# Performance work log

Measured on AMD Instinct MI355X. Metric: run time of the kernel, lower is better.

Reference implementation:

```python
import jax, jax.numpy as jnp
import numpy as np

N_GRAPHS = 500
CHAIN = 200
D_STATE = 64
HID = 128
NEG_SLOPE = 0.2  # PyG GATConv default


def setup_inputs() -> dict:
    key = jax.random.key(0)
    ks = jax.random.split(key, 9)
    N = N_GRAPHS * CHAIN
    # batched bidirectional chain graphs (as in create_chain_graph_batch)
    off = np.arange(N_GRAPHS, dtype=np.int32) * CHAIN
    a = (off[:, None] + np.arange(CHAIN - 1, dtype=np.int32)[None, :]).ravel()
    b = a + 1
    edge_index = jnp.asarray(np.stack([np.concatenate([a, b]), np.concatenate([b, a])]), dtype=jnp.int32)
    x = jax.random.normal(ks[0], (N, D_STATE), jnp.float32)
    s1 = 1.0 / np.sqrt(D_STATE)
    W1 = jax.random.normal(ks[1], (D_STATE, 2 * HID), jnp.float32) * s1
    att_src1 = jax.random.normal(ks[2], (2, HID), jnp.float32) * (1.0 / np.sqrt(HID))
    att_dst1 = jax.random.normal(ks[3], (2, HID), jnp.float32) * (1.0 / np.sqrt(HID))
    b1 = jnp.zeros((2 * HID,), jnp.float32)
    s2 = 1.0 / np.sqrt(2 * HID)
    W2 = jax.random.normal(ks[4], (2 * HID, HID), jnp.float32) * s2
    att_src2 = jax.random.normal(ks[5], (1, HID), jnp.float32) * (1.0 / np.sqrt(HID))
    att_dst2 = jax.random.normal(ks[6], (1, HID), jnp.float32) * (1.0 / np.sqrt(HID))
    b2 = jnp.zeros((HID,), jnp.float32)
    return {"x": x, "edge_index": edge_index, "W1": W1, "att_src1": att_src1,
            "att_dst1": att_dst1, "b1": b1, "W2": W2, "att_src2": att_src2,
            "att_dst2": att_dst2, "b2": b2}


def gat_conv(x, src, dst, W, att_src, att_dst, bias, concat):
    # PyG GATConv: per-head linear, additive attention, segment softmax over dst
    N = x.shape[0]
    H, C = att_src.shape
    h = (x @ W).reshape(N, H, C)                          # [N,H,C]
    a_s = (h * att_src).sum(-1)                           # [N,H]
    a_d = (h * att_dst).sum(-1)                           # [N,H]
    logits = jax.nn.leaky_relu(a_s[src] + a_d[dst], NEG_SLOPE)  # [E,H]
    m = jax.ops.segment_max(logits, dst, num_segments=N)
    e = jnp.exp(logits - m[dst])
    s = jax.ops.segment_sum(e, dst, num_segments=N)
    alpha = e / (s[dst] + 1e-16)                          # [E,H]
    out = jax.ops.segment_sum(h[src] * alpha[:, :, None], dst, num_segments=N)  # [N,H,C]
    out = out.reshape(N, H * C) if concat else out.mean(axis=1)
    return out + bias


def reference(x, edge_index, W1, att_src1, att_dst1, b1, W2, att_src2, att_dst2, b2):
    N = x.shape[0]
    loop = jnp.arange(N, dtype=edge_index.dtype)
    src = jnp.concatenate([edge_index[0], loop])  # add_self_loops=True (PyG default)
    dst = jnp.concatenate([edge_index[1], loop])
    h = gat_conv(x, src, dst, W1, att_src1, att_dst1, b1, concat=True)
    h = jax.nn.gelu(h, approximate=False)  # torch F.gelu default = exact erf
    h = gat_conv(h, src, dst, W2, att_src2, att_dst2, b2, concat=False)
    return jax.nn.gelu(h, approximate=False)
```

## Files before the change

kernel.cpp:

```cpp
#include <hip/hip_runtime.h>
#include <hip/hip_bf16.h>

#define NG 500
#define CH 200
#define NN (NG*CH)
#define DS 64
#define HDIM 128
#define C1 256
#define NEG_SLOPE 0.2f
#define GB 1563

typedef unsigned short ushort_t;
typedef __attribute__((ext_vector_type(8))) short bf16x8;
typedef __attribute__((ext_vector_type(4))) float f32x4;

__device__ __forceinline__ float us2f(ushort_t u){
  union { unsigned int i; float f; } v; v.i = ((unsigned int)u) << 16; return v.f;
}
__device__ __forceinline__ ushort_t f2us(float f){
  union { float f; unsigned int i; } v; v.f = f;
  unsigned int x = v.i;
  return (ushort_t)((x + 0x7fffu + ((x >> 16) & 1u)) >> 16);
}
__device__ __forceinline__ float lrelu(float v){ return v > 0.f ? v : NEG_SLOPE * v; }
__device__ __forceinline__ float gelu_fast(float x){
  float x2 = x * x;
  float z  = x * fmaf(0.0713548162726f, x2, 1.59576912161f);
  float e  = __expf(-z);
  return x / fmaf(e, 1.f, 1.f) ;
}

__global__ void probe_dtype(const void* __restrict__ x, int* __restrict__ flag){
  __shared__ int cnt;
  if (threadIdx.x == 0) cnt = 0;
  __syncthreads();
  const ushort_t* p = (const ushort_t*)x;
  int local = 0;
  for (int i = threadIdx.x; i < 8192; i += 256) {
    float v = us2f(p[i]);
    if (!(fabsf(v) < 100.f)) local++;
  }
  atomicAdd(&cnt, local);
  __syncthreads();
  if (threadIdx.x == 0) flag[0] = (cnt > 16) ? 1 : 0;
}

__global__ void prep_w(const int* __restrict__ flag,
                       const void* W1, const void* as1, const void* ad1, const void* b1,
                       const void* W2, const void* as2, const void* ad2, const void* b2,
                       ushort_t* w1t, ushort_t* w2t,
                       float* asrc1f, float* adst1f, float* b1f,
                       float* asrc2f, float* adst2f, float* b2f)
{
  const bool F = flag[0] != 0;
  int i = blockIdx.x * 256 + threadIdx.x;
  #define LD(p, j) (F ? ((const float*)(p))[j] : us2f(((const ushort_t*)(p))[j]))
  if (i < 16384)      { int k = i >> 8, n = i & 255; w1t[n*64  + k] = f2us(LD(W1, i)); }
  else if (i < 49152) { int j = i - 16384, k = j >> 7, n = j & 127; w2t[n*256 + k] = f2us(LD(W2, j)); }
  else if (i < 49408) { asrc1f[i-49152] = LD(as1, i-49152); }
  else if (i < 49664) { adst1f[i-49408] = LD(ad1, i-49408); }
  else if (i < 49920) { b1f[i-49664]    = LD(b1,  i-49664); }
  else if (i < 50048) { asrc2f[i-49920] = LD(as2, i-49920); }
  else if (i < 50176) { adst2f[i-50048] = LD(ad2, i-50048); }
  else if (i < 50304) { b2f[i-50176]    = LD(b2,  i-50176); }
  #undef LD
}

__global__ __launch_bounds__(256, 4) void fused(
    const int* __restrict__ flag, const void* __restrict__ x,
    const ushort_t* __restrict__ w1t, const ushort_t* __restrict__ w2t,
    const float* __restrict__ asrc1f, const float* __restrict__ adst1f, const float* __restrict__ b1f,
    const float* __restrict__ asrc2f, const float* __restrict__ adst2f, const float* __restrict__ b2f,
    void* __restrict__ out)
{
  __shared__ ushort_t lds[17952];
  __shared__ float part_s[4][68], part_d[4][68];
  __shared__ float alp[66*8];
  ushort_t* As  = lds;
  ushort_t* g1L = lds;

  const int t  = threadIdx.x;
  const int m0 = blockIdx.x * 64;
  const int l = t & 63, w = t >> 6;
  const int ln = l & 15, quad = l >> 4;
  const bool F = flag[0] != 0;

  #pragma unroll
  for (int i = 0; i < 5; i++) {
    int q = t + i*256;
    int r = q >> 4, off = (q & 15) * 4;
    int gr = m0 - 2 + r;
    ushort4 v = {0,0,0,0};
    if (r < 68 && gr >= 0 && gr < NN) {
      if (F) {
        float4 xv = *(const float4*)(&((const float*)x)[(size_t)gr*DS + off]);
        v.x = f2us(xv.x); v.y = f2us(xv.y); v.z = f2us(xv.z); v.w = f2us(xv.w);
      } else {
        v = *(const ushort4*)(&((const ushort_t*)x)[(size_t)gr*DS + off]);
      }
    }
    *(ushort4*)(&As[r*72 + off]) = v;
  }

  f32x4 acc[5][4];
  #pragma unroll
  for (int mi = 0; mi < 5; mi++)
    #pragma unroll
    for (int nj = 0; nj < 4; nj++) acc[mi][nj] = (f32x4){0.f,0.f,0.f,0.f};

  __syncthreads();
  #pragma unroll
  for (int h = 0; h < 2; h++) {
    #pragma unroll
    for (int ks = 0; ks < 2; ks++) {
      const int kk = ks*32 + quad*8;
      bf16x8 a[5], b[2];
      #pragma unroll
      for (int njl = 0; njl < 2; njl++)
        b[njl] = *(const bf16x8*)(&w1t[(w*64 + h*32 + njl*16 + ln)*64 + kk]);
      #pragma unroll
      for (int mi = 0; mi < 5; mi++) a[mi] = *(const bf16x8*)(&As[(mi*16 + ln)*72 + kk]);
      #pragma unroll
      for (int mi = 0; mi < 5; mi++)
        #pragma unroll
        for (int njl = 0; njl < 2; njl++)
          acc[mi][2*h+njl] = __builtin_amdgcn_mfma_f32_16x16x32_bf16(a[mi], b[njl], acc[mi][2*h+njl], 0, 0, 0);
    }
  }

  {
    float wsv[4], wdv[4];
    #pragma unroll
    for (int nj = 0; nj < 4; nj++) {
      wsv[nj] = asrc1f[w*64 + nj*16 + ln];
      wdv[nj] = adst1f[w*64 + nj*16 + ln];
    }
    #pragma unroll
    for (int mi = 0; mi < 5; mi++)
      #pragma unroll
      for (int r = 0; r < 4; r++) {
        float s = 0.f, d = 0.f;
        #pragma unroll
        for (int nj = 0; nj < 4; nj++) { s += acc[mi][nj][r] * wsv[nj]; d += acc[mi][nj][r] * wdv[nj]; }
        #pragma unroll
        for (int o = 1; o < 16; o <<= 1) { s += __shfl_xor(s, o, 64); d += __shfl_xor(d, o, 64); }
        int row = mi*16 + quad*4 + r;
        if (ln == 0 && row < 68) { part_s[w][row] = s; part_d[w][row] = d; }
      }
  }
  __syncthreads();

  if (t < 132) {
    int hh = (t >= 66) ? 1 : 0;
    int n  = t - 66*hh;
    int gj = m0 - 1 + n;
    int p  = gj % CH;
    float ad   = part_d[2*hh][n+1] + part_d[2*hh+1][n+1];
    float as_s = part_s[2*hh][n+1] + part_s[2*hh+1][n+1];
    float as_l = part_s[2*hh][n  ] + part_s[2*hh+1][n  ];
    float as_r = part_s[2*hh][n+2] + part_s[2*hh+1][n+2];
    bool hl = p > 0, hr = p < CH-1;
    float zs = lrelu(as_s + ad);
    float zl = hl ? lrelu(as_l + ad) : -1e30f;
    float zr = hr ? lrelu(as_r + ad) : -1e30f;
    float mx = fmaxf(zs, fmaxf(zl, zr));
    float el = hl ? __expf(zl - mx) : 0.f;
    float es = __expf(zs - mx);
    float er = hr ? __expf(zr - mx) : 0.f;
    float inv = 1.f / (el + es + er + 1e-16f);
    alp[n*8 + hh*4 + 0] = el*inv; alp[n*8 + hh*4 + 1] = es*inv; alp[n*8 + hh*4 + 2] = er*inv;
  }
  __syncthreads();

  {
    float b1v[4];
    #pragma unroll
    for (int nj = 0; nj < 4; nj++) b1v[nj] = b1f[w*64 + nj*16 + ln];
    if (t < 132) {
      int rr = (t < 66) ? 0 : 67;
      int c4 = ((t < 66) ? t : t - 66) * 4;
      ushort4 z = {0,0,0,0};
      *(ushort4*)(&g1L[rr*264 + c4]) = z;
    }
    const int head = w >> 1;
    #pragma unroll
    for (int mi = 0; mi < 5; mi++) {
      const int mip = (mi < 4) ? mi+1 : 4;
      const int mim = (mi > 0) ? mi-1 : 0;
      float hp3[4], hm0[4];
      #pragma unroll
      for (int nj = 0; nj < 4; nj++) {
        float up_a = __shfl(acc[mi ][nj][0], (l+16)&63, 64);
        float up_b = __shfl(acc[mip][nj][0], (l+16)&63, 64);
        float dn_a = __shfl(acc[mi ][nj][3], (l-16)&63, 64);
        float dn_b = __shfl(acc[mim][nj][3], (l-16)&63, 64);
        hp3[nj] = (quad < 3) ? up_a : up_b;
        hm0[nj] = (quad > 0) ? dn_a : dn_b;
      }
      #pragma unroll
      for (int r = 0; r < 4; r++) {
        int row = mi*16 + quad*4 + r;
        if (row >= 1 && row <= 66) {
          float4 av = *(const float4*)(&alp[(row-1)*8 + head*4]);
          #pragma unroll
          for (int nj = 0; nj < 4; nj++) {
            float self = acc[mi][nj][r];
            float hm = (r > 0) ? acc[mi][nj][r-1] : hm0[nj];
            float hp = (r < 3) ? acc[mi][nj][r+1] : hp3[nj];
            float v = av.y*self + av.x*hm + av.z*hp + b1v[nj];
            g1L[row*264 + w*64 + nj*16 + ln] = f2us(gelu_fast(v));
          }
        }
      }
    }
  }
  __syncthreads();

  f32x4 acc2[5][2];
  #pragma unroll
  for (int mi = 0; mi < 5; mi++)
    #pragma unroll
    for (int nj = 0; nj < 2; nj++) acc2[mi][nj] = (f32x4){0.f,0.f,0.f,0.f};

  #pragma unroll
  for (int ck = 0; ck < 4; ck++) {
    bf16x8 a2[2][5];
    #pragma unroll
    for (int ks = 0; ks < 2; ks++)
      #pragma unroll
      for (int mi = 0; mi < 5; mi++) {
        int ar = mi*16 + ln;
        if (mi == 4) ar = (ar < 67) ? ar : 67;
        a2[ks][mi] = *(const bf16x8*)(&g1L[ar*264 + ck*64 + ks*32 + quad*8]);
      }
    #pragma unroll
    for (int h2 = 0; h2 < 2; h2++) {
      #pragma unroll
      for (int ks = 0; ks < 2; ks++) {
        bf16x8 b = *(const bf16x8*)(&w2t[(w*32 + h2*16 + ln)*256 + ck*64 + ks*32 + quad*8]);
        #pragma unroll
        for (int mi = 0; mi < 5; mi++)
          acc2[mi][h2] = __builtin_amdgcn_mfma_f32_16x16x32_bf16(a2[ks][mi], b, acc2[mi][h2], 0, 0, 0);
      }
    }
  }

  {
    float ws2[2], wd2[2];
    #pragma unroll
    for (int nj = 0; nj < 2; nj++) {
      ws2[nj] = asrc2f[w*32 + nj*16 + ln];
      wd2[nj] = adst2f[w*32 + nj*16 + ln];
    }
    #pragma unroll
    for (int mi = 0; mi < 5; mi++)
      #pragma unroll
      for (int r = 0; r < 4; r++) {
        float s = 0.f, d = 0.f;
        #pragma unroll
        for (int nj = 0; nj < 2; nj++) { s += acc2[mi][nj][r] * ws2[nj]; d += acc2[mi][nj][r] * wd2[nj]; }
        #pragma unroll
        for (int o = 1; o < 16; o <<= 1) { s += __shfl_xor(s, o, 64); d += __shfl_xor(d, o, 64); }
        int row = mi*16 + quad*4 + r;
        if (ln == 0 && row < 68) { part_s[w][row] = s; part_d[w][row] = d; }
      }
  }
  __syncthreads();

  if (t < 64) {
    int gi = m0 + t;
    if (gi < NN) {
      int p = gi % CH;
      float ad = 0.f, as_s = 0.f, as_l = 0.f, as_r = 0.f;
      #pragma unroll
      for (int ww = 0; ww < 4; ww++) {
        ad   += part_d[ww][t+2];
        as_s += part_s[ww][t+2];
        as_l += part_s[ww][t+1];
        as_r += part_s[ww][t+3];
      }
      bool hl = p > 0, hr = p < CH-1;
      float zs = lrelu(as_s + ad);
      float zl = hl ? lrelu(as_l + ad) : -1e30f;
      float zr = hr ? lrelu(as_r + ad) : -1e30f;
      float mx = fmaxf(zs, fmaxf(zl, zr));
      float el = hl ? __expf(zl - mx) : 0.f;
      float es = __expf(zs - mx);
      float er = hr ? __expf(zr - mx) : 0.f;
      float inv = 1.f / (el + es + er + 1e-16f);
      alp[t*4 + 0] = el*inv; alp[t*4 + 1] = es*inv; alp[t*4 + 2] = er*inv;
    }
  }
  __syncthreads();

  {
    float b2v[2];
    #pragma unroll
    for (int nj = 0; nj < 2; nj++) b2v[nj] = b2f[w*32 + nj*16 + ln];
    #pragma unroll
    for (int mi = 0; mi < 5; mi++) {
      const int mip = (mi < 4) ? mi+1 : 4;
      const int mim = (mi > 0) ? mi-1 : 0;
      float hp3[2], hm0[2];
      #pragma unroll
      for (int nj = 0; nj < 2; nj++) {
        float up_a = __shfl(acc2[mi ][nj][0], (l+16)&63, 64);
        float up_b = __shfl(acc2[mip][nj][0], (l+16)&63, 64);
        float dn_a = __shfl(acc2[mi ][nj][3], (l-16)&63, 64);
        float dn_b = __shfl(acc2[mim][nj][3], (l-16)&63, 64);
        hp3[nj] = (quad < 3) ? up_a : up_b;
        hm0[nj] = (quad > 0) ? dn_a : dn_b;
      }
      #pragma unroll
      for (int r = 0; r < 4; r++) {
        int row = mi*16 + quad*4 + r;
        if (row >= 2 && row <= 65) {
          int n = row - 2;
          int gi = m0 + n;
          if (gi < NN) {
            float4 av = *(const float4*)(&alp[n*4]);
            #pragma unroll
            for (int nj = 0; nj < 2; nj++) {
              float self = acc2[mi][nj][r];
              float hm = (r > 0) ? acc2[mi][nj][r-1] : hm0[nj];
              float hp = (r < 3) ? acc2[mi][nj][r+1] : hp3[nj];
              float v = av.y*self + av.x*hm + av.z*hp + b2v[nj];
              float o = gelu_fast(v);
              int c2 = w*32 + nj*16 + ln;
              if (F) ((float*)out)[(size_t)gi*HDIM + c2] = o;
              else   ((ushort_t*)out)[(size_t)gi*HDIM + c2] = f2us(o);
            }
          }
        }
      }
    }
  }
}

extern "C" void kernel_launch(void* const* d_in, const int* in_sizes, int n_in,
                              void* d_out, int out_size, void* d_ws, size_t ws_size,
                              hipStream_t stream)
{
  const void* x   = d_in[0];
  const void* W1  = d_in[2];
  const void* as1 = d_in[3];
  const void* ad1 = d_in[4];
  const void* b1  = d_in[5];
  const void* W2  = d_in[6];
  const void* as2 = d_in[7];
  const void* ad2 = d_in[8];
  const void* b2  = d_in[9];

  char* w = (char*)d_ws;
  size_t off = 0;
  int* flag = (int*)w;                       off += 256;
  ushort_t* w1t = (ushort_t*)(w + off);      off += 64 * 256 * 2;
  ushort_t* w2t = (ushort_t*)(w + off);      off += 256 * 128 * 2;
  float* asrc1f = (float*)(w + off);         off += 256 * 4;
  float* adst1f = (float*)(w + off);         off += 256 * 4;
  float* b1f    = (float*)(w + off);         off += 256 * 4;
  float* asrc2f = (float*)(w + off);         off += 128 * 4;
  float* adst2f = (float*)(w + off);         off += 128 * 4;
  float* b2f    = (float*)(w + off);         off += 128 * 4;

  probe_dtype<<<1, 256, 0, stream>>>(x, flag);
  prep_w<<<197, 256, 0, stream>>>(flag, W1, as1, ad1, b1, W2, as2, ad2, b2,
                                  w1t, w2t, asrc1f, adst1f, b1f, asrc2f, adst2f, b2f);
  fused<<<GB, 256, 0, stream>>>(flag, x, w1t, w2t, asrc1f, adst1f, b1f,
                                asrc2f, adst2f, b2f, d_out);
}
```

Measured before the change: 173.6 us.

## Fold attention vectors into weights and compute attention logits via extra MFMA

Precomputes W·att_src and W·att_dst vectors, split into hi/lo bf16 pairs, in the prep kernel. The fused kernel then gets per-node attention logits from an extra MFMA column tile instead of per-lane dot products plus a 16-lane shuffle reduction, and the LDS partial arrays are merged into one scratch buffer. It also uses packed bf16 conversion instructions, rcp intrinsics and a reworked gelu. The trade is extra MFMA work on one wave per K-slice, plus a small precision change from the bf16 hi/lo split and the approximate reciprocal.

```diff
diff --git a/kernel.cpp b/kernel.cpp
--- a/kernel.cpp
+++ b/kernel.cpp
@@ -22,12 +22,17 @@
   unsigned int x = v.i;
   return (ushort_t)((x + 0x7fffu + ((x >> 16) & 1u)) >> 16);
 }
+__device__ __forceinline__ unsigned int cvt_pk_bf16(float a, float b){
+  unsigned int r;
+  asm("v_cvt_pk_bf16_f32 %0, %1, %2" : "=v"(r) : "v"(a), "v"(b));
+  return r;
+}
 __device__ __forceinline__ float lrelu(float v){ return v > 0.f ? v : NEG_SLOPE * v; }
 __device__ __forceinline__ float gelu_fast(float x){
   float x2 = x * x;
-  float z  = x * fmaf(0.0713548162726f, x2, 1.59576912161f);
-  float e  = __expf(-z);
-  return x / fmaf(e, 1.f, 1.f) ;
+  float zn = x * fmaf(-0.0713548163f, x2, -1.5957691216f);
+  float e  = __expf(zn);
+  return x * __builtin_amdgcn_rcpf(1.f + e);
 }
 
 __global__ void probe_dtype(const void* __restrict__ x, int* __restrict__ flag){
@@ -50,7 +55,8 @@
                        const void* W2, const void* as2, const void* ad2, const void* b2,
                        ushort_t* w1t, ushort_t* w2t,
                        float* asrc1f, float* adst1f, float* b1f,
-                       float* asrc2f, float* adst2f, float* b2f)
+                       float* asrc2f, float* adst2f, float* b2f,
+                       ushort_t* wsd1, ushort_t* wsd2)
 {
   const bool F = flag[0] != 0;
   int i = blockIdx.x * 256 + threadIdx.x;
@@ -63,19 +69,41 @@
   else if (i < 50048) { asrc2f[i-49920] = LD(as2, i-49920); }
   else if (i < 50176) { adst2f[i-50048] = LD(ad2, i-50048); }
   else if (i < 50304) { b2f[i-50176]    = LD(b2,  i-50176); }
+  else if (i < 50560) {
+    int j = i - 50304, k = j >> 2, c = j & 3;
+    int head = c >> 1;
+    const void* av = (c & 1) ? ad1 : as1;
+    float s = 0.f;
+    for (int cc = 0; cc < 128; cc++)
+      s += LD(W1, k*256 + head*128 + cc) * LD(av, head*128 + cc);
+    ushort_t hi = f2us(s);
+    wsd1[c*64 + k] = hi;
+    wsd1[(c+4)*64 + k] = f2us(s - us2f(hi));
+  }
+  else if (i < 51072) {
+    int j = i - 50560, k = j >> 1, c = j & 1;
+    const void* av = c ? ad2 : as2;
+    float s = 0.f;
+    for (int cc = 0; cc < 128; cc++)
+      s += LD(W2, k*128 + cc) * LD(av, cc);
+    ushort_t hi = f2us(s);
+    wsd2[c*256 + k] = hi;
+    wsd2[(c+2)*256 + k] = f2us(s - us2f(hi));
+  }
+  else if (i < 51584) { wsd1[512  + (i - 51072)] = 0; }
+  else if (i < 54656) { wsd2[1024 + (i - 51584)] = 0; }
   #undef LD
 }
 
 __global__ __launch_bounds__(256, 4) void fused(
     const int* __restrict__ flag, const void* __restrict__ x,
     const ushort_t* __restrict__ w1t, const ushort_t* __restrict__ w2t,
-    const float* __restrict__ asrc1f, const float* __restrict__ adst1f, const float* __restrict__ b1f,
-    const float* __restrict__ asrc2f, const float* __restrict__ adst2f, const float* __restrict__ b2f,
+    const ushort_t* __restrict__ wsd1, const ushort_t* __restrict__ wsd2,
+    const float* __restrict__ b1f, const float* __restrict__ b2f,
     void* __restrict__ out)
 {
   __shared__ ushort_t lds[17952];
-  __shared__ float part_s[4][68], part_d[4][68];
-  __shared__ float alp[66*8];
+  __shared__ float scratch[800];
   ushort_t* As  = lds;
   ushort_t* g1L = lds;
 
@@ -90,16 +118,18 @@
     int q = t + i*256;
     int r = q >> 4, off = (q & 15) * 4;
     int gr = m0 - 2 + r;
-    ushort4 v = {0,0,0,0};
     if (r < 68 && gr >= 0 && gr < NN) {
       if (F) {
         float4 xv = *(const float4*)(&((const float*)x)[(size_t)gr*DS + off]);
-        v.x = f2us(xv.x); v.y = f2us(xv.y); v.z = f2us(xv.z); v.w = f2us(xv.w);
+        uint2 u; u.x = cvt_pk_bf16(xv.x, xv.y); u.y = cvt_pk_bf16(xv.z, xv.w);
+        *(uint2*)(&As[r*72 + off]) = u;
       } else {
-        v = *(const ushort4*)(&((const ushort_t*)x)[(size_t)gr*DS + off]);
-      }
-    }
-    *(ushort4*)(&As[r*72 + off]) = v;
+        *(ushort4*)(&As[r*72 + off]) = *(const ushort4*)(&((const ushort_t*)x)[(size_t)gr*DS + off]);
+      }
+    } else {
+      ushort4 z = {0,0,0,0};
+      *(ushort4*)(&As[r*72 + off]) = z;
+    }
   }
 
   f32x4 acc[5][4];
@@ -107,6 +137,9 @@
   for (int mi = 0; mi < 5; mi++)
     #pragma unroll
     for (int nj = 0; nj < 4; nj++) acc[mi][nj] = (f32x4){0.f,0.f,0.f,0.f};
+  f32x4 acc_att[5];
+  #pragma unroll
+  for (int mi = 0; mi < 5; mi++) acc_att[mi] = (f32x4){0.f,0.f,0.f,0.f};
 
   __syncthreads();
   #pragma unroll
@@ -125,27 +158,24 @@
         #pragma unroll
         for (int njl = 0; njl < 2; njl++)
           acc[mi][2*h+njl] = __builtin_amdgcn_mfma_f32_16x16x32_bf16(a[mi], b[njl], acc[mi][2*h+njl], 0, 0, 0);
-    }
-  }
-
-  {
-    float wsv[4], wdv[4];
-    #pragma unroll
-    for (int nj = 0; nj < 4; nj++) {
-      wsv[nj] = asrc1f[w*64 + nj*16 + ln];
-      wdv[nj] = adst1f[w*64 + nj*16 + ln];
-    }
+      if (h == 0 && w == 0) {
+        bf16x8 batt = *(const bf16x8*)(&wsd1[ln*64 + kk]);
+        #pragma unroll
+        for (int mi = 0; mi < 5; mi++)
+          acc_att[mi] = __builtin_amdgcn_mfma_f32_16x16x32_bf16(a[mi], batt, acc_att[mi], 0, 0, 0);
+      }
+    }
+  }
+
+  if (w == 0) {
     #pragma unroll
     for (int mi = 0; mi < 5; mi++)
       #pragma unroll
       for (int r = 0; r < 4; r++) {
-        float s = 0.f, d = 0.f;
-        #pragma unroll
-        for (int nj = 0; nj < 4; nj++) { s += acc[mi][nj][r] * wsv[nj]; d += acc[mi][nj][r] * wdv[nj]; }
-        #pragma unroll
-        for (int o = 1; o < 16; o <<= 1) { s += __shfl_xor(s, o, 64); d += __shfl_xor(d, o, 64); }
+        float v = acc_att[mi][r];
+        float vc = v + __shfl(v, (l + 4) & 63, 64);
         int row = mi*16 + quad*4 + r;
-        if (ln == 0 && row < 68) { part_s[w][row] = s; part_d[w][row] = d; }
+        if (ln < 4 && row < 68) scratch[ln*68 + row] = vc;
       }
   }
   __syncthreads();
@@ -155,10 +185,9 @@
     int n  = t - 66*hh;
     int gj = m0 - 1 + n;
     int p  = gj % CH;
-    float ad   = part_d[2*hh][n+1] + part_d[2*hh+1][n+1];
-    float as_s = part_s[2*hh][n+1] + part_s[2*hh+1][n+1];
-    float as_l = part_s[2*hh][n  ] + part_s[2*hh+1][n  ];
-    float as_r = part_s[2*hh][n+2] + part_s[2*hh+1][n+2];
+    const float* Sa = &scratch[(2*hh)*68];
+    const float* Da = &scratch[(2*hh+1)*68];
+    float ad = Da[n+1], as_s = Sa[n+1], as_l = Sa[n], as_r = Sa[n+2];
     bool hl = p > 0, hr = p < CH-1;
     float zs = lrelu(as_s + ad);
     float zl = hl ? lrelu(as_l + ad) : -1e30f;
@@ -167,8 +196,10 @@
     float el = hl ? __expf(zl - mx) : 0.f;
     float es = __expf(zs - mx);
     float er = hr ? __expf(zr - mx) : 0.f;
-    float inv = 1.f / (el + es + er + 1e-16f);
-    alp[n*8 + hh*4 + 0] = el*inv; alp[n*8 + hh*4 + 1] = es*inv; alp[n*8 + hh*4 + 2] = er*inv;
+    float inv = __builtin_amdgcn_rcpf(el + es + er + 1e-16f);
+    scratch[272 + n*8 + hh*4 + 0] = el*inv;
+    scratch[272 + n*8 + hh*4 + 1] = es*inv;
+    scratch[272 + n*8 + hh*4 + 2] = er*inv;
   }
   __syncthreads();
 
@@ -176,9 +207,9 @@
     float b1v[4];
     #pragma unroll
     for (int nj = 0; nj < 4; nj++) b1v[nj] = b1f[w*64 + nj*16 + ln];
-    if (t < 132) {
-      int rr = (t < 66) ? 0 : 67;
-      int c4 = ((t < 66) ? t : t - 66) * 4;
+    if (t < 128) {
+      int rr = (t < 64) ? 0 : 67;
+      int c4 = (t & 63) * 4;
       ushort4 z = {0,0,0,0};
       *(ushort4*)(&g1L[rr*264 + c4]) = z;
     }
@@ -201,15 +232,20 @@
       for (int r = 0; r < 4; r++) {
         int row = mi*16 + quad*4 + r;
         if (row >= 1 && row <= 66) {
-          float4 av = *(const float4*)(&alp[(row-1)*8 + head*4]);
+          float4 av = *(const float4*)(&scratch[272 + (row-1)*8 + head*4]);
+          float o[4];
           #pragma unroll
           for (int nj = 0; nj < 4; nj++) {
             float self = acc[mi][nj][r];
             float hm = (r > 0) ? acc[mi][nj][r-1] : hm0[nj];
             float hp = (r < 3) ? acc[mi][nj][r+1] : hp3[nj];
-            float v = av.y*self + av.x*hm + av.z*hp + b1v[nj];
-            g1L[row*264 + w*64 + nj*16 + ln] = f2us(gelu_fast(v));
+            o[nj] = gelu_fast(av.y*self + av.x*hm + av.z*hp + b1v[nj]);
           }
+          unsigned int u01 = cvt_pk_bf16(o[0], o[1]);
+          unsigned int u23 = cvt_pk_bf16(o[2], o[3]);
+          ushort_t* base = &g1L[row*264 + w*64 + ln];
+          base[0]  = (ushort_t)u01; base[16] = (ushort_t)(u01 >> 16);
+          base[32] = (ushort_t)u23; base[48] = (ushort_t)(u23 >> 16);
         }
       }
     }
@@ -221,6 +257,9 @@
   for (int mi = 0; mi < 5; mi++)
     #pragma unroll
     for (int nj = 0; nj < 2; nj++) acc2[mi][nj] = (f32x4){0.f,0.f,0.f,0.f};
+  f32x4 acc2_att[5];
+  #pragma unroll
+  for (int mi = 0; mi < 5; mi++) acc2_att[mi] = (f32x4){0.f,0.f,0.f,0.f};
 
   #pragma unroll
   for (int ck = 0; ck < 4; ck++) {
@@ -233,6 +272,15 @@
         if (mi == 4) ar = (ar < 67) ? ar : 67;
         a2[ks][mi] = *(const bf16x8*)(&g1L[ar*264 + ck*64 + ks*32 + quad*8]);
       }
+    if (ck == w) {
+      #pragma unroll
+      for (int ks = 0; ks < 2; ks++) {
+        bf16x8 batt2 = *(const bf16x8*)(&wsd2[ln*256 + ck*64 + ks*32 + quad*8]);
+        #pragma unroll
+        for (int mi = 0; mi < 5; mi++)
+          acc2_att[mi] = __builtin_amdgcn_mfma_f32_16x16x32_bf16(a2[ks][mi], batt2, acc2_att[mi], 0, 0, 0);
+      }
+    }
     #pragma unroll
     for (int h2 = 0; h2 < 2; h2++) {
       #pragma unroll
@@ -245,26 +293,15 @@
     }
   }
 
-  {
-    float ws2[2], wd2[2];
-    #pragma unroll
-    for (int nj = 0; nj < 2; nj++) {
-      ws2[nj] = asrc2f[w*32 + nj*16 + ln];
-      wd2[nj] = adst2f[w*32 + nj*16 + ln];
-    }
-    #pragma unroll
-    for (int mi = 0; mi < 5; mi++)
-      #pragma unroll
-      for (int r = 0; r < 4; r++) {
-        float s = 0.f, d = 0.f;
-        #pragma unroll
-        for (int nj = 0; nj < 2; nj++) { s += acc2[mi][nj][r] * ws2[nj]; d += acc2[mi][nj][r] * wd2[nj]; }
-        #pragma unroll
-        for (int o = 1; o < 16; o <<= 1) { s += __shfl_xor(s, o, 64); d += __shfl_xor(d, o, 64); }
-        int row = mi*16 + quad*4 + r;
-        if (ln == 0 && row < 68) { part_s[w][row] = s; part_d[w][row] = d; }
-      }
-  }
+  #pragma unroll
+  for (int mi = 0; mi < 5; mi++)
+    #pragma unroll
+    for (int r = 0; r < 4; r++) {
+      float v = acc2_att[mi][r];
+      float vc = v + __shfl(v, (l + 2) & 63, 64);
+      int row = mi*16 + quad*4 + r;
+      if (ln < 2 && row < 68) scratch[(w*2 + ln)*68 + row] = vc;
+    }
   __syncthreads();
 
   if (t < 64) {
@@ -274,10 +311,10 @@
       float ad = 0.f, as_s = 0.f, as_l = 0.f, as_r = 0.f;
       #pragma unroll
       for (int ww = 0; ww < 4; ww++) {
-        ad   += part_d[ww][t+2];
-        as_s += part_s[ww][t+2];
-        as_l += part_s[ww][t+1];
-        as_r += part_s[ww][t+3];
+        as_s += scratch[(ww*2)*68 + t+2];
+        as_l += scratch[(ww*2)*68 + t+1];
+        as_r += scratch[(ww*2)*68 + t+3];
+        ad   += scratch[(ww*2+1)*68 + t+2];
       }
       bool hl = p > 0, hr = p < CH-1;
       float zs = lrelu(as_s + ad);
@@ -287,8 +324,10 @@
       float el = hl ? __expf(zl - mx) : 0.f;
       float es = __expf(zs - mx);
       float er = hr ? __expf(zr - mx) : 0.f;
-      float inv = 1.f / (el + es + er + 1e-16f);
-      alp[t*4 + 0] = el*inv; alp[t*4 + 1] = es*inv; alp[t*4 + 2] = er*inv;
+      float inv = __builtin_amdgcn_rcpf(el + es + er + 1e-16f);
+      scratch[544 + t*4 + 0] = el*inv;
+      scratch[544 + t*4 + 1] = es*inv;
+      scratch[544 + t*4 + 2] = er*inv;
     }
   }
   __syncthreads();
@@ -318,17 +357,28 @@
           int n = row - 2;
           int gi = m0 + n;
           if (gi < NN) {
-            float4 av = *(const float4*)(&alp[n*4]);
-            #pragma unroll
-            for (int nj = 0; nj < 2; nj++) {
-              float self = acc2[mi][nj][r];
-              float hm = (r > 0) ? acc2[mi][nj][r-1] : hm0[nj];
-              float hp = (r < 3) ? acc2[mi][nj][r+1] : hp3[nj];
-              float v = av.y*self + av.x*hm + av.z*hp + b2v[nj];
-              float o = gelu_fast(v);
-              int c2 = w*32 + nj*16 + ln;
-              if (F) ((float*)out)[(size_t)gi*HDIM + c2] = o;
-              else   ((ushort_t*)out)[(size_t)gi*HDIM + c2] = f2us(o);
+            float4 av = *(const float4*)(&scratch[544 + n*4]);
+            float o0, o1;
+            {
+              float self = acc2[mi][0][r];
+              float hm = (r > 0) ? acc2[mi][0][r-1] : hm0[0];
+              float hp = (r < 3) ? acc2[mi][0][r+1] : hp3[0];
+              o0 = gelu_fast(av.y*self + av.x*hm + av.z*hp + b2v[0]);
+            }
+            {
+              float self = acc2[mi][1][r];
+              float hm = (r > 0) ? acc2[mi][1][r-1] : hm0[1];
+              float hp = (r < 3) ? acc2[mi][1][r+1] : hp3[1];
+              o1 = gelu_fast(av.y*self + av.x*hm + av.z*hp + b2v[1]);
+            }
+            int c2 = w*32 + ln;
+            if (F) {
+              ((float*)out)[(size_t)gi*HDIM + c2]      = o0;
+              ((float*)out)[(size_t)gi*HDIM + c2 + 16] = o1;
+            } else {
+              unsigned int u = cvt_pk_bf16(o0, o1);
+              ((ushort_t*)out)[(size_t)gi*HDIM + c2]      = (ushort_t)u;
+              ((ushort_t*)out)[(size_t)gi*HDIM + c2 + 16] = (ushort_t)(u >> 16);
             }
           }
         }
@@ -362,10 +412,12 @@
   float* asrc2f = (float*)(w + off);         off += 128 * 4;
   float* adst2f = (float*)(w + off);         off += 128 * 4;
   float* b2f    = (float*)(w + off);         off += 128 * 4;
+  ushort_t* wsd1 = (ushort_t*)(w + off);     off += 16 * 64 * 2;
+  ushort_t* wsd2 = (ushort_t*)(w + off);     off += 16 * 256 * 2;
 
   probe_dtype<<<1, 256, 0, stream>>>(x, flag);
-  prep_w<<<197, 256, 0, stream>>>(flag, W1, as1, ad1, b1, W2, as2, ad2, b2,
-                                  w1t, w2t, asrc1f, adst1f, b1f, asrc2f, adst2f, b2f);
-  fused<<<GB, 256, 0, stream>>>(flag, x, w1t, w2t, asrc1f, adst1f, b1f,
-                                asrc2f, adst2f, b2f, d_out);
-}
+  prep_w<<<214, 256, 0, stream>>>(flag, W1, as1, ad1, b1, W2, as2, ad2, b2,
+                                  w1t, w2t, asrc1f, adst1f, b1f, asrc2f, adst2f, b2f,
+                                  wsd1, wsd2);
+  fused<<<GB, 256, 0, stream>>>(flag, x, w1t, w2t, wsd1, wsd2, b1f, b2f, d_out);
+}
```

Result: slower. 177.9 us (+2.5%).
